# Optimization experiments

Measured on AMD Instinct MI355X. Metric: run time of the kernel, lower is better.

## Reference

```python
import jax, jax.numpy as jnp
import numpy as np

B, D, H, K = 65536, 256, 256, 11
TEMP = 1.0
EPS = 1e-8  # torch cosine_similarity eps


def _gelu(v):
    return jax.nn.gelu(v, approximate=False)  # torch nn.GELU default is exact


def setup_inputs() -> dict:
    key = jax.random.key(0)
    ks = jax.random.split(key, 9)
    s_d = 1.0 / np.sqrt(D)
    s_h = 1.0 / np.sqrt(H)
    return {
        "x": jax.random.normal(ks[0], (B, D), jnp.float32),
        # K transform MLPs, stacked: D->H (gelu) ->D
        "Tw1": jax.random.normal(ks[1], (K, D, H), jnp.float32) * s_d,
        "Tb1": jax.random.normal(ks[2], (K, H), jnp.float32) * 0.01,
        "Tw2": jax.random.normal(ks[3], (K, H, D), jnp.float32) * s_h,
        "Tb2": jax.random.normal(ks[4], (K, D), jnp.float32) * 0.01,
        # encoder MLP: D->H (gelu) ->H
        "Ew1": jax.random.normal(ks[5], (D, H), jnp.float32) * s_d,
        "Eb1": jax.random.normal(ks[6], (H,), jnp.float32) * 0.01,
        "Ew2": jax.random.normal(ks[7], (H, H), jnp.float32) * s_h,
        "Eb2": jax.random.normal(ks[8], (H,), jnp.float32) * 0.01,
    }


def reference(x, Tw1, Tb1, Tw2, Tb2, Ew1, Eb1, Ew2, Eb2):
    def enc(h):  # [..., D] -> [..., H]; dropout is identity at inference
        return _gelu(h @ Ew1 + Eb1) @ Ew2 + Eb2

    # batched transforms: [K, B, D]
    tx = _gelu(jnp.einsum('bd,kdh->kbh', x, Tw1) + Tb1[:, None, :])
    tx = jnp.einsum('kbh,khd->kbd', tx, Tw2) + Tb2[:, None, :]

    z = enc(x)        # [B, H]
    zt = enc(tx)      # [K, B, H]

    nz = jnp.linalg.norm(z, axis=-1)    # [B]
    nzt = jnp.linalg.norm(zt, axis=-1)  # [K, B]

    # exp(cos(z, z_k) / T)  -> [K, B]
    sim_z = jnp.exp(jnp.einsum('bh,kbh->kb', z, zt)
                    / jnp.maximum(nz[None, :] * nzt, EPS) / TEMP)
    # exp(cos(z_l, z_k) / T) -> [K, K, B]
    S = jnp.exp(jnp.einsum('lbh,kbh->lkb', zt, zt)
                / jnp.maximum(nzt[:, None, :] * nzt[None, :, :], EPS) / TEMP)
    diag = jnp.diagonal(S, axis1=0, axis2=1).T  # [K, B]
    neg = S.sum(axis=0) - diag                  # sum over l != k

    scores = jnp.log(sim_z / (sim_z + neg))     # [K, B]
    return -scores.sum(axis=0)                  # [B]
```

## Files before the change

kernel.cpp:

```cpp
#include <hip/hip_runtime.h>
#include <hip/hip_bf16.h>
#include <stdint.h>

#define BTOT  65536
#define KTR   11
#define NSLOT 12

typedef __attribute__((ext_vector_type(8))) short bf16x8_t;
typedef __attribute__((ext_vector_type(4))) float f32x4_t;

__device__ __forceinline__ int act_addr(int m, int n) {
    return m * 256 + ((((n >> 3) + m) & 31) << 3) + (n & 7);
}

__device__ __forceinline__ float gelu_fast(float x) {
    float x2 = x * x;
    float t2 = 2.3022083f * x * fmaf(0.044715f, x2, 1.0f);
    float e  = exp2f(fminf(t2, 44.f));
    return x * e * __builtin_amdgcn_rcpf(1.0f + e);
}

__global__ void cast_x_kernel(const float* __restrict__ x, __hip_bfloat16* __restrict__ xb) {
    int i = (blockIdx.x * 256 + threadIdx.x) * 4;
    float4 v = *(const float4*)(x + i);
    union { __hip_bfloat16 h[4]; uint64_t u; } o;
    o.h[0] = __float2bfloat16(v.x);
    o.h[1] = __float2bfloat16(v.y);
    o.h[2] = __float2bfloat16(v.z);
    o.h[3] = __float2bfloat16(v.w);
    *(uint64_t*)(xb + i) = o.u;
}

__global__ void transpose_cast_kernel(const float* __restrict__ in,
                                      __hip_bfloat16* __restrict__ out,
                                      int R, int C) {
    __shared__ float tile[32][33];
    int tpc = C >> 5;
    int tr = (blockIdx.x / tpc) << 5;
    int tc = (blockIdx.x % tpc) << 5;
    const float* bi = in + (size_t)blockIdx.y * R * C;
    __hip_bfloat16* bo = out + (size_t)blockIdx.y * R * C;
    int lx = threadIdx.x & 31, ly = threadIdx.x >> 5;
    #pragma unroll
    for (int r = 0; r < 32; r += 8)
        tile[ly + r][lx] = bi[(size_t)(tr + ly + r) * C + tc + lx];
    __syncthreads();
    #pragma unroll
    for (int r = 0; r < 32; r += 8)
        bo[(size_t)(tc + ly + r) * R + tr + lx] = __float2bfloat16(tile[lx][ly + r]);
}

__global__ void fuse_w_kernel(const __hip_bfloat16* __restrict__ Ew1t,
                              const __hip_bfloat16* __restrict__ Tw2b,
                              __hip_bfloat16* __restrict__ Wft)
{
    __shared__ __align__(16) __hip_bfloat16 bt[64 * 256];
    const int tid  = threadIdx.x;
    const int wave = tid >> 6, lane = tid & 63;
    const int lr = lane & 15, q = lane >> 4;
    const int k  = blockIdx.y;
    const int h0 = blockIdx.x << 6;
    const __hip_bfloat16* src = Tw2b + (size_t)k * 65536;

    #pragma unroll
    for (int i = 0; i < 8; ++i) {
        int lin = i * 256 + tid;
        int r = lin >> 5, g = lin & 31;
        bf16x8_t v = *(const bf16x8_t*)(src + (size_t)(h0 + r) * 256 + g * 8);
        *(bf16x8_t*)(bt + act_addr(r, g * 8)) = v;
    }
    __syncthreads();

    const int wc = wave << 6;
    f32x4_t acc[4][4];
    #pragma unroll
    for (int mt = 0; mt < 4; ++mt)
        #pragma unroll
        for (int nt = 0; nt < 4; ++nt)
            acc[mt][nt] = (f32x4_t){0.f, 0.f, 0.f, 0.f};

    #pragma unroll 1
    for (int kc = 0; kc < 8; ++kc) {
        const int kof = (kc << 5) + (q << 3);
        bf16x8_t a[4], b[4];
        #pragma unroll
        for (int mt = 0; mt < 4; ++mt)
            a[mt] = *(const bf16x8_t*)(Ew1t + (size_t)(wc + (mt << 4) + lr) * 256 + kof);
        #pragma unroll
        for (int nt = 0; nt < 4; ++nt)
            b[nt] = *(const bf16x8_t*)(bt + act_addr((nt << 4) + lr, kof));
        #pragma unroll
        for (int mt = 0; mt < 4; ++mt)
            #pragma unroll
            for (int nt = 0; nt < 4; ++nt)
                acc[mt][nt] = __builtin_amdgcn_mfma_f32_16x16x32_bf16(a[mt], b[nt], acc[mt][nt], 0, 0, 0);
    }

    __hip_bfloat16* dst = Wft + (size_t)k * 65536;
    #pragma unroll
    for (int mt = 0; mt < 4; ++mt)
        #pragma unroll
        for (int nt = 0; nt < 4; ++nt) {
            const int h = h0 + (nt << 4) + lr;
            #pragma unroll
            for (int r = 0; r < 4; ++r) {
                const int j = wc + (mt << 4) + (q << 2) + r;
                dst[(size_t)j * 256 + h] = __float2bfloat16(acc[mt][nt][r]);
            }
        }
}

__global__ void fuse_b_kernel(const float* __restrict__ Tb2,
                              const float* __restrict__ Ew1,
                              const float* __restrict__ Eb1,
                              float* __restrict__ bf)
{
    const int k = blockIdx.x, j = threadIdx.x;
    float s = Eb1[j];
    #pragma unroll 4
    for (int d = 0; d < 256; ++d)
        s = fmaf(Tb2[k * 256 + d], Ew1[d * 256 + j], s);
    bf[k * 256 + j] = s;
}

template<bool DO_GELU>
__device__ void run_stage(__hip_bfloat16* act,
                          const __hip_bfloat16* __restrict__ Wt,
                          const float* __restrict__ bias,
                          int wave, int lane)
{
    const int lr = lane & 15;
    const int q  = lane >> 4;
    const int wc = wave << 6;

    f32x4_t acc[4][4];
    #pragma unroll
    for (int mt = 0; mt < 4; ++mt) {
        const float4 bv = *(const float4*)(bias + wc + (mt << 4) + (q << 2));
        #pragma unroll
        for (int nt = 0; nt < 4; ++nt)
            acc[mt][nt] = (f32x4_t){bv.x, bv.y, bv.z, bv.w};
    }

    bf16x8_t a[4];
    #pragma unroll
    for (int mt = 0; mt < 4; ++mt)
        a[mt] = *(const bf16x8_t*)(Wt + (size_t)(wc + (mt << 4) + lr) * 256 + (q << 3));

    #pragma unroll 1
    for (int kc = 0; kc < 8; ++kc) {
        const int kof = (kc << 5) + (q << 3);
        bf16x8_t an[4];
        if (kc < 7) {
            #pragma unroll
            for (int mt = 0; mt < 4; ++mt)
                an[mt] = *(const bf16x8_t*)(Wt + (size_t)(wc + (mt << 4) + lr) * 256 + kof + 32);
        }
        bf16x8_t b[4];
        #pragma unroll
        for (int nt = 0; nt < 4; ++nt)
            b[nt] = *(const bf16x8_t*)(act + act_addr((nt << 4) + lr, kof));
        #pragma unroll
        for (int mt = 0; mt < 4; ++mt)
            #pragma unroll
            for (int nt = 0; nt < 4; ++nt)
                acc[mt][nt] = __builtin_amdgcn_mfma_f32_16x16x32_bf16(a[mt], b[nt], acc[mt][nt], 0, 0, 0);
        if (kc < 7) {
            #pragma unroll
            for (int mt = 0; mt < 4; ++mt) a[mt] = an[mt];
        }
    }

    __syncthreads();
    #pragma unroll
    for (int mt = 0; mt < 4; ++mt) {
        const int nbase = wc + (mt << 4) + (q << 2);
        #pragma unroll
        for (int nt = 0; nt < 4; ++nt) {
            const int row = (nt << 4) + lr;
            union { __hip_bfloat16 h[4]; uint64_t u; } o;
            #pragma unroll
            for (int r = 0; r < 4; ++r) {
                float v = acc[mt][nt][r];
                if (DO_GELU) v = gelu_fast(v);
                o.h[r] = __float2bfloat16(v);
            }
            *(uint64_t*)(act + act_addr(row, nbase)) = o.u;
        }
    }
    __syncthreads();
}

__launch_bounds__(256, 3)
__global__ void chain_kernel(const __hip_bfloat16* __restrict__ xb,
                             const __hip_bfloat16* __restrict__ Tw1t,
                             const float* __restrict__ Tb1,
                             const __hip_bfloat16* __restrict__ Wft,
                             const float* __restrict__ bfb,
                             const __hip_bfloat16* __restrict__ Ew1t,
                             const float* __restrict__ Eb1,
                             const __hip_bfloat16* __restrict__ Ew2t,
                             const float* __restrict__ Eb2,
                             __hip_bfloat16* __restrict__ zbuf,
                             int b0)
{
    __shared__ __align__(16) __hip_bfloat16 act[64 * 256];
    const int tid  = threadIdx.x;
    const int wave = tid >> 6, lane = tid & 63;
    const int slot = blockIdx.y;
    const int tile = blockIdx.x;

    #pragma unroll
    for (int i = 0; i < 8; ++i) {
        int lin = i * 256 + tid;
        int r = lin >> 5, g = lin & 31;
        bf16x8_t v = *(const bf16x8_t*)(xb + (size_t)(b0 + tile * 64 + r) * 256 + g * 8);
        *(bf16x8_t*)(act + act_addr(r, g * 8)) = v;
    }
    __syncthreads();

    if (slot < KTR) {
        run_stage<true>(act, Tw1t + (size_t)slot * 65536, Tb1 + slot * 256, wave, lane);
        run_stage<true>(act, Wft  + (size_t)slot * 65536, bfb + slot * 256, wave, lane);
    } else {
        run_stage<true>(act, Ew1t, Eb1, wave, lane);
    }
    run_stage<false>(act, Ew2t, Eb2, wave, lane);

    __hip_bfloat16* dst = zbuf + (size_t)(tile * NSLOT + slot) * (64 * 256);
    #pragma unroll
    for (int i = 0; i < 8; ++i) {
        int lin = i * 256 + tid;
        int r = lin >> 5, g = lin & 31;
        bf16x8_t v = *(const bf16x8_t*)(act + act_addr(r, g * 8));
        __builtin_nontemporal_store(v, (bf16x8_t*)(dst + lin * 8));
    }
}

#define ROW_BODY(V, I)                                                        \
    {                                                                         \
        f32x4_t acc = (f32x4_t){0.f, 0.f, 0.f, 0.f};                          \
        _Pragma("unroll")                                                     \
        for (int kc = 0; kc < 8; ++kc)                                        \
            acc = __builtin_amdgcn_mfma_f32_16x16x32_bf16(V[kc], V[kc], acc, 0, 0, 0); \
        _Pragma("unroll")                                                     \
        for (int rr = 0; rr < 4; ++rr)                                        \
            Gw[wave][(q << 2) + rr][lr] = acc[rr];                            \
        float term = 0.f;                                                     \
        if (lane < 11) {                                                      \
            const int k = lane;                                               \
            float nr[NSLOT];                                                  \
            _Pragma("unroll")                                                 \
            for (int l = 0; l < NSLOT; ++l)                                   \
                nr[l] = __builtin_amdgcn_rcpf(fmaxf(sqrtf(Gw[wave][l][l]), 1e-4f)); \
            const float nrk = nr[k];                                          \
            float neg = 0.f;                                                  \
            _Pragma("unroll")                                                 \
            for (int l = 0; l < KTR; ++l)                                     \
                if (l != k)                                                   \
                    neg += __expf(Gw[wave][l][k] * nr[l] * nrk);              \
            float cz = Gw[wave][KTR][k] * nr[KTR] * nrk;                      \
            term = __logf(__expf(cz) + neg) - cz;                             \
        }                                                                     \
        term += __shfl_xor(term, 1);                                          \
        term += __shfl_xor(term, 2);                                          \
        term += __shfl_xor(term, 4);                                          \
        term += __shfl_xor(term, 8);                                          \
        if (lane == 0) out[b0 + r0 + (I)] = term;                             \
    }

__launch_bounds__(256, 4)
__global__ void reduce_kernel(const __hip_bfloat16* __restrict__ zbuf,
                              float* __restrict__ out, int b0)
{
    __shared__ float Gw[4][16][17];
    const int tid  = threadIdx.x;
    const int wave = tid >> 6, lane = tid & 63;
    const int lr = lane & 15, q = lane >> 4;
    const int slot = lr < NSLOT ? lr : NSLOT - 1;

    const int r0   = (blockIdx.x * 4 + wave) * 8;
    const int tile = r0 >> 6, rloc = r0 & 63;
    const __hip_bfloat16* zr = zbuf + (size_t)tile * (NSLOT * 64 * 256)
                             + (size_t)slot * (64 * 256) + rloc * 256 + (q << 3);

    bf16x8_t va[8], vb[8];
    #pragma unroll
    for (int kc = 0; kc < 8; ++kc)
        va[kc] = __builtin_nontemporal_load((const bf16x8_t*)(zr + kc * 32));

    #pragma unroll 1
    for (int i2 = 0; i2 < 4; ++i2) {
        const int ie = i2 * 2;
        {
            const __hip_bfloat16* zn = zr + (ie + 1) * 256;
            #pragma unroll
            for (int kc = 0; kc < 8; ++kc)
                vb[kc] = __builtin_nontemporal_load((const bf16x8_t*)(zn + kc * 32));
            ROW_BODY(va, ie)
        }
        {
            if (ie + 2 < 8) {
                const __hip_bfloat16* zn = zr + (ie + 2) * 256;
                #pragma unroll
                for (int kc = 0; kc < 8; ++kc)
                    va[kc] = __builtin_nontemporal_load((const bf16x8_t*)(zn + kc * 32));
            }
            ROW_BODY(vb, ie + 1)
        }
    }
}

extern "C" void kernel_launch(void* const* d_in, const int* in_sizes, int n_in,
                              void* d_out, int out_size, void* d_ws, size_t ws_size,
                              hipStream_t stream)
{
    const float* x   = (const float*)d_in[0];
    const float* Tw1 = (const float*)d_in[1];
    const float* Tb1 = (const float*)d_in[2];
    const float* Tw2 = (const float*)d_in[3];
    const float* Tb2 = (const float*)d_in[4];
    const float* Ew1 = (const float*)d_in[5];
    const float* Eb1 = (const float*)d_in[6];
    const float* Ew2 = (const float*)d_in[7];
    const float* Eb2 = (const float*)d_in[8];
    float* out = (float*)d_out;

    char* ws = (char*)d_ws;
    const size_t off_xb   = 0;
    const size_t off_tw1  = off_xb   + (size_t)BTOT * 256 * 2;
    const size_t off_wf   = off_tw1  + (size_t)KTR * 65536 * 2;
    const size_t off_ew1  = off_wf   + (size_t)KTR * 65536 * 2;
    const size_t off_ew2  = off_ew1  + (size_t)65536 * 2;
    const size_t off_tw2b = off_ew2  + (size_t)65536 * 2;
    const size_t off_bf   = off_tw2b + (size_t)KTR * 65536 * 2;
    const size_t off_z    = off_bf   + (size_t)KTR * 256 * 4;

    __hip_bfloat16* xb   = (__hip_bfloat16*)(ws + off_xb);
    __hip_bfloat16* Tw1t = (__hip_bfloat16*)(ws + off_tw1);
    __hip_bfloat16* Wft  = (__hip_bfloat16*)(ws + off_wf);
    __hip_bfloat16* Ew1t = (__hip_bfloat16*)(ws + off_ew1);
    __hip_bfloat16* Ew2t = (__hip_bfloat16*)(ws + off_ew2);
    __hip_bfloat16* Tw2b = (__hip_bfloat16*)(ws + off_tw2b);
    float*          bfb  = (float*)(ws + off_bf);
    __hip_bfloat16* zbuf = (__hip_bfloat16*)(ws + off_z);

    long long zbytes = (long long)ws_size - (long long)off_z;
    long long rows_cap = zbytes > 0 ? zbytes / ((long long)NSLOT * 256 * 2) : 0;
    int chunk = (int)((rows_cap / 128) * 128);
    if (chunk > BTOT / 4) chunk = BTOT / 4;
    if (chunk < 128) chunk = 128;

    cast_x_kernel<<<dim3(BTOT * 256 / 1024), 256, 0, stream>>>(x, xb);
    cast_x_kernel<<<dim3(KTR * 65536 / 1024), 256, 0, stream>>>(Tw2, Tw2b);
    transpose_cast_kernel<<<dim3(64, KTR), 256, 0, stream>>>(Tw1, Tw1t, 256, 256);
    transpose_cast_kernel<<<dim3(64, 1),   256, 0, stream>>>(Ew1, Ew1t, 256, 256);
    transpose_cast_kernel<<<dim3(64, 1),   256, 0, stream>>>(Ew2, Ew2t, 256, 256);
    fuse_b_kernel<<<dim3(KTR), 256, 0, stream>>>(Tb2, Ew1, Eb1, bfb);
    fuse_w_kernel<<<dim3(4, KTR), 256, 0, stream>>>(Ew1t, Tw2b, Wft);

    for (int b0 = 0; b0 < BTOT; b0 += chunk) {
        int rows = (BTOT - b0 < chunk) ? (BTOT - b0) : chunk;
        chain_kernel<<<dim3(rows / 64, NSLOT), 256, 0, stream>>>(
            xb, Tw1t, Tb1, Wft, bfb, Ew1t, Eb1, Ew2t, Eb2, zbuf, b0);
        reduce_kernel<<<dim3(rows / 32), 256, 0, stream>>>(zbuf, out, b0);
    }
}
```

Measured before the change: 867.8 us.

## Process two slots per block, interleaving MFMA of one with epilogue of other

```diff
diff --git a/kernel.cpp b/kernel.cpp
--- a/kernel.cpp
+++ b/kernel.cpp
@@ -16,8 +16,8 @@
 __device__ __forceinline__ float gelu_fast(float x) {
     float x2 = x * x;
     float t2 = 2.3022083f * x * fmaf(0.044715f, x2, 1.0f);
-    float e  = exp2f(fminf(t2, 44.f));
-    return x * e * __builtin_amdgcn_rcpf(1.0f + e);
+    float e  = exp2f(-t2);
+    return x * __builtin_amdgcn_rcpf(1.0f + e);
 }
 
 __global__ void cast_x_kernel(const float* __restrict__ x, __hip_bfloat16* __restrict__ xb) {
@@ -123,17 +123,11 @@
     bf[k * 256 + j] = s;
 }
 
-template<bool DO_GELU>
-__device__ void run_stage(__hip_bfloat16* act,
-                          const __hip_bfloat16* __restrict__ Wt,
-                          const float* __restrict__ bias,
-                          int wave, int lane)
-{
-    const int lr = lane & 15;
-    const int q  = lane >> 4;
-    const int wc = wave << 6;
-
-    f32x4_t acc[4][4];
+__device__ __forceinline__ void mfma_part(const __hip_bfloat16* act,
+                                          const __hip_bfloat16* __restrict__ Wt,
+                                          const float* __restrict__ bias,
+                                          f32x4_t acc[4][4], int lr, int q, int wc)
+{
     #pragma unroll
     for (int mt = 0; mt < 4; ++mt) {
         const float4 bv = *(const float4*)(bias + wc + (mt << 4) + (q << 2));
@@ -141,22 +135,13 @@
         for (int nt = 0; nt < 4; ++nt)
             acc[mt][nt] = (f32x4_t){bv.x, bv.y, bv.z, bv.w};
     }
-
-    bf16x8_t a[4];
-    #pragma unroll
-    for (int mt = 0; mt < 4; ++mt)
-        a[mt] = *(const bf16x8_t*)(Wt + (size_t)(wc + (mt << 4) + lr) * 256 + (q << 3));
-
     #pragma unroll 1
     for (int kc = 0; kc < 8; ++kc) {
         const int kof = (kc << 5) + (q << 3);
-        bf16x8_t an[4];
-        if (kc < 7) {
-            #pragma unroll
-            for (int mt = 0; mt < 4; ++mt)
-                an[mt] = *(const bf16x8_t*)(Wt + (size_t)(wc + (mt << 4) + lr) * 256 + kof + 32);
-        }
-        bf16x8_t b[4];
+        bf16x8_t a[4], b[4];
+        #pragma unroll
+        for (int mt = 0; mt < 4; ++mt)
+            a[mt] = *(const bf16x8_t*)(Wt + (size_t)(wc + (mt << 4) + lr) * 256 + kof);
         #pragma unroll
         for (int nt = 0; nt < 4; ++nt)
             b[nt] = *(const bf16x8_t*)(act + act_addr((nt << 4) + lr, kof));
@@ -165,13 +150,13 @@
             #pragma unroll
             for (int nt = 0; nt < 4; ++nt)
                 acc[mt][nt] = __builtin_amdgcn_mfma_f32_16x16x32_bf16(a[mt], b[nt], acc[mt][nt], 0, 0, 0);
-        if (kc < 7) {
-            #pragma unroll
-            for (int mt = 0; mt < 4; ++mt) a[mt] = an[mt];
-        }
-    }
-
-    __syncthreads();
+    }
+}
+
+template<bool DO_GELU>
+__device__ __forceinline__ void ep_part(__hip_bfloat16* act, f32x4_t acc[4][4],
+                                        int lr, int q, int wc)
+{
     #pragma unroll
     for (int mt = 0; mt < 4; ++mt) {
         const int nbase = wc + (mt << 4) + (q << 2);
@@ -188,10 +173,9 @@
             *(uint64_t*)(act + act_addr(row, nbase)) = o.u;
         }
     }
-    __syncthreads();
-}
-
-__launch_bounds__(256, 3)
+}
+
+__launch_bounds__(256, 2)
 __global__ void chain_kernel(const __hip_bfloat16* __restrict__ xb,
                              const __hip_bfloat16* __restrict__ Tw1t,
                              const float* __restrict__ Tb1,
@@ -204,36 +188,70 @@
                              __hip_bfloat16* __restrict__ zbuf,
                              int b0)
 {
-    __shared__ __align__(16) __hip_bfloat16 act[64 * 256];
+    __shared__ __align__(16) __hip_bfloat16 actA[64 * 256];
+    __shared__ __align__(16) __hip_bfloat16 actB[64 * 256];
     const int tid  = threadIdx.x;
     const int wave = tid >> 6, lane = tid & 63;
-    const int slot = blockIdx.y;
+    const int lr = lane & 15, q = lane >> 4, wc = wave << 6;
+    const int pair = blockIdx.y;
     const int tile = blockIdx.x;
+    const int s0 = pair * 2, s1 = s0 + 1;
+    const bool zp = (pair == 5);
 
     #pragma unroll
     for (int i = 0; i < 8; ++i) {
         int lin = i * 256 + tid;
         int r = lin >> 5, g = lin & 31;
         bf16x8_t v = *(const bf16x8_t*)(xb + (size_t)(b0 + tile * 64 + r) * 256 + g * 8);
-        *(bf16x8_t*)(act + act_addr(r, g * 8)) = v;
-    }
-    __syncthreads();
-
-    if (slot < KTR) {
-        run_stage<true>(act, Tw1t + (size_t)slot * 65536, Tb1 + slot * 256, wave, lane);
-        run_stage<true>(act, Wft  + (size_t)slot * 65536, bfb + slot * 256, wave, lane);
-    } else {
-        run_stage<true>(act, Ew1t, Eb1, wave, lane);
-    }
-    run_stage<false>(act, Ew2t, Eb2, wave, lane);
-
-    __hip_bfloat16* dst = zbuf + (size_t)(tile * NSLOT + slot) * (64 * 256);
+        *(bf16x8_t*)(actA + act_addr(r, g * 8)) = v;
+        *(bf16x8_t*)(actB + act_addr(r, g * 8)) = v;
+    }
+    __syncthreads();
+
+    const __hip_bfloat16* WA0 = Tw1t + (size_t)s0 * 65536;
+    const __hip_bfloat16* WA1 = Wft  + (size_t)s0 * 65536;
+    const float* BA0 = Tb1 + s0 * 256;
+    const float* BA1 = bfb + s0 * 256;
+    const __hip_bfloat16* WB0 = zp ? Ew1t : Tw1t + (size_t)s1 * 65536;
+    const __hip_bfloat16* WB1 = zp ? Ew2t : Wft  + (size_t)s1 * 65536;
+    const float* BB0 = zp ? Eb1 : Tb1 + s1 * 256;
+    const float* BB1 = zp ? Eb2 : bfb + s1 * 256;
+
+    f32x4_t accA[4][4], accB[4][4];
+
+    mfma_part(actA, WA0, BA0, accA, lr, q, wc);
+    __syncthreads();
+    mfma_part(actB, WB0, BB0, accB, lr, q, wc);
+    ep_part<true>(actA, accA, lr, q, wc);
+    __syncthreads();
+    mfma_part(actA, WA1, BA1, accA, lr, q, wc);
+    ep_part<true>(actB, accB, lr, q, wc);
+    __syncthreads();
+    mfma_part(actB, WB1, BB1, accB, lr, q, wc);
+    ep_part<true>(actA, accA, lr, q, wc);
+    __syncthreads();
+    mfma_part(actA, Ew2t, Eb2, accA, lr, q, wc);
+    if (zp) ep_part<false>(actB, accB, lr, q, wc);
+    else    ep_part<true >(actB, accB, lr, q, wc);
+    __syncthreads();
+    if (!zp) mfma_part(actB, Ew2t, Eb2, accB, lr, q, wc);
+    ep_part<false>(actA, accA, lr, q, wc);
+    __syncthreads();
+    if (!zp) {
+        ep_part<false>(actB, accB, lr, q, wc);
+        __syncthreads();
+    }
+
+    __hip_bfloat16* d0 = zbuf + (size_t)(tile * NSLOT + s0) * (64 * 256);
+    __hip_bfloat16* d1 = zbuf + (size_t)(tile * NSLOT + s1) * (64 * 256);
     #pragma unroll
     for (int i = 0; i < 8; ++i) {
         int lin = i * 256 + tid;
         int r = lin >> 5, g = lin & 31;
-        bf16x8_t v = *(const bf16x8_t*)(act + act_addr(r, g * 8));
-        __builtin_nontemporal_store(v, (bf16x8_t*)(dst + lin * 8));
+        bf16x8_t v0 = *(const bf16x8_t*)(actA + act_addr(r, g * 8));
+        __builtin_nontemporal_store(v0, (bf16x8_t*)(d0 + lin * 8));
+        bf16x8_t v1 = *(const bf16x8_t*)(actB + act_addr(r, g * 8));
+        __builtin_nontemporal_store(v1, (bf16x8_t*)(d1 + lin * 8));
     }
 }
 
@@ -361,7 +379,7 @@
 
     for (int b0 = 0; b0 < BTOT; b0 += chunk) {
         int rows = (BTOT - b0 < chunk) ? (BTOT - b0) : chunk;
-        chain_kernel<<<dim3(rows / 64, NSLOT), 256, 0, stream>>>(
+        chain_kernel<<<dim3(rows / 64, NSLOT / 2), 256, 0, stream>>>(
             xb, Tw1t, Tb1, Wft, bfb, Ew1t, Eb1, Ew2t, Eb2, zbuf, b0);
         reduce_kernel<<<dim3(rows / 32), 256, 0, stream>>>(zbuf, out, b0);
     }
```

Result: faster. 838.4 us (-3.4%).
